# Kernel tuning notes

Measured on AMD Instinct MI355X. Metric: run time of the kernel, lower is better.

## Reference

```python
import jax, jax.numpy as jnp
import numpy as np

WS = 8          # window_size
NH = 8          # num_heads
VD = 512        # values_dim
CD = 128        # coords_dim
INNER = 512     # inner_ratio * values_dim
E = INNER // NH # head_dim = 64
B, Hh, Ww_ = 2, 224, 224

# relative position indices (static)
_idx = np.array([[x, y] for x in range(WS) for y in range(WS)])
_rel = _idx[None, :, :] - _idx[:, None, :] + WS - 1  # (WS^2, WS^2, 2)
REL0 = jnp.asarray(_rel[:, :, 0])
REL1 = jnp.asarray(_rel[:, :, 1])

# shifted-window masks (static)
_s = WS * (WS // 2)
_rm = np.zeros((WS * WS, WS * WS), np.float32)
_rm[-_s:, :-_s] = -np.inf
_rm[:-_s, -_s:] = -np.inf
_cm = _rm.reshape(WS, WS, WS, WS).transpose(1, 0, 3, 2).reshape(WS * WS, WS * WS)
ROW_MASK = jnp.asarray(_rm)
COL_MASK = jnp.asarray(_cm)


def _rmsnorm(x, g, eps=1e-6):
    return x * g * jax.lax.rsqrt(jnp.mean(x * x, axis=-1, keepdims=True) + eps)


def _to_windows(x, b, Wh, Ww):
    # x: (b, hp, wp, INNER) with channel layout (e H) (head fastest)
    x = x.reshape(b, Wh, WS, Ww, WS, E, NH)
    return x.transpose(0, 6, 1, 3, 2, 4, 5).reshape(b, NH, Wh, Ww, WS * WS, E)


def setup_inputs() -> dict:
    key = jax.random.key(0)
    ks = jax.random.split(key, 8)
    s = 0.02
    return {
        "embedded_values": jax.random.normal(ks[0], (B, Hh, Ww_, VD), jnp.float32),
        "embedded_coords": jax.random.normal(ks[1], (B, Hh, Ww_, CD), jnp.float32),
        "Wqk_v": jax.random.normal(ks[2], (VD, 2 * INNER), jnp.float32) * s,
        "bqk_v": jnp.zeros((2 * INNER,), jnp.float32),
        "g_v": jnp.ones((2 * INNER,), jnp.float32),
        "Wv": jax.random.normal(ks[3], (VD, INNER), jnp.float32) * s,
        "bv": jnp.zeros((INNER,), jnp.float32),
        "Wqk_c": jax.random.normal(ks[4], (CD, 2 * INNER), jnp.float32) * s,
        "bqk_c": jnp.zeros((2 * INNER,), jnp.float32),
        "g_c": jnp.ones((2 * INNER,), jnp.float32),
        "pos_emb": jax.random.normal(ks[5], (2 * WS - 1, 2 * WS - 1), jnp.float32),
        "Wout": jax.random.normal(ks[6], (INNER, VD), jnp.float32) * s,
        "bout": jnp.zeros((VD,), jnp.float32),
    }


def reference(embedded_values, embedded_coords, Wqk_v, bqk_v, g_v, Wv, bv,
              Wqk_c, bqk_c, g_c, pos_emb, Wout, bout):
    b, h, w, _ = embedded_values.shape
    # projections; torch concat then rearrange '(d k)' k=3 interleaves channels -> reshape (..., INNER, 3)
    vqk = _rmsnorm(embedded_values @ Wqk_v + bqk_v, g_v)          # (b,h,w,2*INNER)
    vval = embedded_values @ Wv + bv                               # (b,h,w,INNER)
    v = jnp.concatenate([vqk, vval], axis=-1).reshape(b, h, w, INNER, 3)
    c = _rmsnorm(embedded_coords @ Wqk_c + bqk_c, g_c).reshape(b, h, w, INNER, 2)

    pad_h = (-h) % WS
    pad_w = (-w) % WS
    v = jnp.pad(v, ((0, 0), (0, pad_h), (0, pad_w), (0, 0), (0, 0)))
    c = jnp.pad(c, ((0, 0), (0, pad_h), (0, pad_w), (0, 0), (0, 0)))
    # shifted=True: roll windows by half window (no inverse roll in original)
    v = jnp.roll(v, (-(WS // 2), -(WS // 2)), axis=(1, 2))
    c = jnp.roll(c, (-(WS // 2), -(WS // 2)), axis=(1, 2))

    hp, wp = h + pad_h, w + pad_w
    Wh, Ww = hp // WS, wp // WS
    qv = _to_windows(v[..., 0], b, Wh, Ww)
    kv = _to_windows(v[..., 1], b, Wh, Ww)
    vv = _to_windows(v[..., 2], b, Wh, Ww)
    qc = _to_windows(c[..., 0], b, Wh, Ww)
    kc = _to_windows(c[..., 1], b, Wh, Ww)

    scale = float(E) ** 0.5
    dots = (jnp.einsum('bhijpe,bhijqe->bhijpq', qv, kv)
            + jnp.einsum('bhijpe,bhijqe->bhijpq', qc, kc)) / scale
    dots = dots + pos_emb[REL0, REL1]
    # shifted-window masks on last window row / column
    dots = dots.at[:, :, -1, :].add(ROW_MASK)
    dots = dots.at[:, :, :, -1].add(COL_MASK)

    attn = jax.nn.softmax(dots, axis=-1)
    y = jnp.einsum('bhijpq,bhijqe->bhijpe', attn, vv)
    # un-window; output channel layout is (H e) (head slow)
    y = y.reshape(b, NH, Wh, Ww, WS, WS, E).transpose(0, 2, 4, 3, 5, 1, 6)
    y = y.reshape(b, hp, wp, INNER)[:, :h, :w, :]
    return y @ Wout + bout
```

## Files before the change

kernel.cpp:

```cpp
#include <hip/hip_runtime.h>


using u16 = unsigned short;
typedef short bf16x8 __attribute__((ext_vector_type(8)));
typedef float f32x4 __attribute__((ext_vector_type(4)));
typedef u16 u16x4 __attribute__((ext_vector_type(4)));
typedef u16 u16x8 __attribute__((ext_vector_type(8)));

__device__ __forceinline__ float bf2f(u16 v) {
  return __uint_as_float(((unsigned)v) << 16);
}
__device__ __forceinline__ u16 f2bf(float f) {
  unsigned u = __float_as_uint(f);
  u += 0x7fffu + ((u >> 16) & 1u);
  return (u16)(u >> 16);
}

__device__ __forceinline__ void gld16(const u16* g, u16* l) {
  __builtin_amdgcn_global_load_lds(
      (const __attribute__((address_space(1))) unsigned*)g,
      (__attribute__((address_space(3))) unsigned*)l, 16, 0, 0);
}

__global__ void conv_bf16(const float* __restrict__ in, u16* __restrict__ out) {
  size_t i = ((size_t)blockIdx.x * 256 + threadIdx.x) * 8;
  float4 a = *(const float4*)(in + i);
  float4 b = *(const float4*)(in + i + 4);
  u16x8 o;
  o[0] = f2bf(a.x); o[1] = f2bf(a.y); o[2] = f2bf(a.z); o[3] = f2bf(a.w);
  o[4] = f2bf(b.x); o[5] = f2bf(b.y); o[6] = f2bf(b.z); o[7] = f2bf(b.w);
  *(u16x8*)(out + i) = o;
}

__global__ void prep_wv(const float* __restrict__ Wqkv, const float* __restrict__ Wv,
                        u16* __restrict__ out) {
  int idx = blockIdx.x * 256 + threadIdx.x;
  if (idx >= 1536 * 512) return;
  int j = idx >> 9, kk = idx & 511;
  int t = j >> 9, rr = j & 511, nn = rr >> 6, e = rr & 63;
  int cc = 3 * (e * 8 + nn) + t;
  float v = (cc < 1024) ? Wqkv[kk * 1024 + cc] : Wv[kk * 512 + (cc - 1024)];
  out[idx] = f2bf(v);
}

__global__ void prep_wc(const float* __restrict__ W, u16* __restrict__ out) {
  int idx = blockIdx.x * 256 + threadIdx.x;
  if (idx >= 1024 * 128) return;
  int j = idx >> 7, kk = idx & 127;
  int t = j >> 9, rr = j & 511, nn = rr >> 6, e = rr & 63;
  int cc = 2 * (e * 8 + nn) + t;
  out[idx] = f2bf(W[kk * 1024 + cc]);
}

__global__ void prep_wout(const float* __restrict__ W, u16* __restrict__ out) {
  int idx = blockIdx.x * 256 + threadIdx.x;
  if (idx >= 512 * 512) return;
  int o = idx >> 9, kk = idx & 511;
  out[idx] = f2bf(W[kk * 512 + o]);
}

__global__ void prep_vec(const float* __restrict__ bqkv, const float* __restrict__ g_v,
                         const float* __restrict__ bv, const float* __restrict__ bqkc,
                         const float* __restrict__ g_c,
                         float* __restrict__ bpv, float* __restrict__ gAv, float* __restrict__ gBv,
                         float* __restrict__ bpc, float* __restrict__ gAc, float* __restrict__ gBc) {
  int j = blockIdx.x * 256 + threadIdx.x;
  if (j < 1536) {
    int t = j >> 9, rr = j & 511, nn = rr >> 6, e = rr & 63;
    int cc = 3 * (e * 8 + nn) + t;
    if (cc < 1024) { bpv[j] = bqkv[cc]; gAv[j] = g_v[cc]; gBv[j] = 0.f; }
    else           { bpv[j] = bv[cc - 1024]; gAv[j] = 0.f; gBv[j] = 1.f; }
  }
  if (j < 1024) {
    int t = j >> 9, rr = j & 511, nn = rr >> 6, e = rr & 63;
    int cc = 2 * (e * 8 + nn) + t;
    bpc[j] = bqkc[cc]; gAc[j] = g_c[cc]; gBc[j] = 0.f;
  }
}

__global__ void prep_biasT(const float* __restrict__ pe, float* __restrict__ bT) {
  int idx = blockIdx.x * 256 + threadIdx.x;
  if (idx >= 4 * 4096) return;
  int v = idx >> 12, q = (idx >> 6) & 63, p = idx & 63;
  int ap = p >> 3, bp = p & 7, aq = q >> 3, bq = q & 7;
  float val = pe[(aq - ap + 7) * 15 + (bq - bp + 7)];
  if ((v & 1) && ((ap >= 4) != (aq >= 4))) val = -1e30f;
  if ((v & 2) && ((bp >= 4) != (bq >= 4))) val = -1e30f;
  bT[idx] = val;
}

template<int N, int K, int MODE>
__global__ __launch_bounds__(256) void gemm_bt(
    const u16* __restrict__ A, const u16* __restrict__ Bt,
    const float* __restrict__ bias, void* __restrict__ outp,
    float* __restrict__ part, const float* __restrict__ gB) {
  constexpr int NCB = N / 128;
  const int bn = blockIdx.x, bm = blockIdx.y;
  const int tid = threadIdx.x;
  const int w = tid >> 6;
  const int lane = tid & 63;
  const int wr = w >> 1, wc = w & 1;
  const int g = lane >> 4, c = lane & 15;

  __shared__ u16 As[128 * 64];
  __shared__ u16 Bs[128 * 64];

  f32x4 acc[4][4] = {};
  const u16* Ag = A + (size_t)bm * 128 * K;
  const u16* Bg = Bt + (size_t)bn * 128 * K;

  const int lr = lane >> 3;
  const int lc = (lane & 7) * 8;

  for (int kt = 0; kt < K / 64; ++kt) {
    const int k0 = kt * 64;
#pragma unroll
    for (int i = 0; i < 4; ++i) {
      const int rbase = (w * 4 + i) * 8;
      gld16(Ag + (size_t)(rbase + lr) * K + k0 + lc, As + rbase * 64 + lane * 8);
      gld16(Bg + (size_t)(rbase + lr) * K + k0 + lc, Bs + rbase * 64 + lane * 8);
    }
    __syncthreads();
#pragma unroll
    for (int kk = 0; kk < 2; ++kk) {
      bf16x8 af[4], bfv[4];
#pragma unroll
      for (int mi = 0; mi < 4; ++mi)
        af[mi] = *(const bf16x8*)(As + (wr * 64 + mi * 16 + c) * 64 + kk * 32 + g * 8);
#pragma unroll
      for (int ni = 0; ni < 4; ++ni)
        bfv[ni] = *(const bf16x8*)(Bs + (wc * 64 + ni * 16 + c) * 64 + kk * 32 + g * 8);
#pragma unroll
      for (int mi = 0; mi < 4; ++mi)
#pragma unroll
        for (int ni = 0; ni < 4; ++ni)
          acc[mi][ni] = __builtin_amdgcn_mfma_f32_16x16x32_bf16(af[mi], bfv[ni], acc[mi][ni], 0, 0, 0);
    }
    __syncthreads();
  }

  const int rowbase = bm * 128 + wr * 64;
  const int colbase = bn * 128 + wc * 64;
  if constexpr (MODE == 0) {
    u16* O = (u16*)outp;
    float rowsq[4][4];
#pragma unroll
    for (int mi = 0; mi < 4; ++mi)
#pragma unroll
      for (int r = 0; r < 4; ++r) rowsq[mi][r] = 0.f;
#pragma unroll
    for (int ni = 0; ni < 4; ++ni) {
      const int col = colbase + ni * 16 + c;
      const float bb = bias[col];
      const float fl = (gB[col] == 0.f) ? 1.f : 0.f;
#pragma unroll
      for (int mi = 0; mi < 4; ++mi)
#pragma unroll
        for (int r = 0; r < 4; ++r) {
          float v = acc[mi][ni][r] + bb;
          O[(size_t)(rowbase + mi * 16 + g * 4 + r) * N + col] = f2bf(v);
          rowsq[mi][r] += fl * v * v;
        }
    }
#pragma unroll
    for (int mi = 0; mi < 4; ++mi)
#pragma unroll
      for (int r = 0; r < 4; ++r) {
        float s = rowsq[mi][r];
        s += __shfl_xor(s, 1); s += __shfl_xor(s, 2);
        s += __shfl_xor(s, 4); s += __shfl_xor(s, 8);
        rowsq[mi][r] = s;
      }
    __syncthreads();
    float* red = (float*)As;
    if (c == 0) {
#pragma unroll
      for (int mi = 0; mi < 4; ++mi)
#pragma unroll
        for (int r = 0; r < 4; ++r)
          red[wc * 128 + wr * 64 + mi * 16 + g * 4 + r] = rowsq[mi][r];
    }
    __syncthreads();
    if (tid < 128)
      part[(size_t)(bm * 128 + tid) * NCB + bn] = red[tid] + red[128 + tid];
  } else {
    float* O = (float*)outp;
#pragma unroll
    for (int ni = 0; ni < 4; ++ni) {
      const int col = colbase + ni * 16 + c;
      const float bb = bias[col];
#pragma unroll
      for (int mi = 0; mi < 4; ++mi)
#pragma unroll
        for (int r = 0; r < 4; ++r)
          O[(size_t)(rowbase + mi * 16 + g * 4 + r) * N + col] = acc[mi][ni][r] + bb;
    }
  }
}

__global__ void combine_scales(const float* __restrict__ pvp, const float* __restrict__ pcp,
                               float* __restrict__ sv, float* __restrict__ sc) {
  const int i = blockIdx.x * 256 + threadIdx.x;
  float s = 0.f;
#pragma unroll
  for (int k = 0; k < 12; ++k) s += pvp[(size_t)i * 12 + k];
  sv[i] = rsqrtf(s * (1.f / 1024.f) + 1e-6f);
  float s2 = 0.f;
#pragma unroll
  for (int k = 0; k < 8; ++k) s2 += pcp[(size_t)i * 8 + k];
  sc[i] = rsqrtf(s2 * (1.f / 1024.f) + 1e-6f);
}

__device__ __forceinline__ void store_norm(u16* dst, u16x8 raw, const float* gA,
                                           const float* gB, float s, int e0) {
  u16x8 o;
#pragma unroll
  for (int j = 0; j < 8; ++j) {
    float fac = gA[e0 + j] * s + gB[e0 + j];
    o[j] = f2bf(bf2f(raw[j]) * fac);
  }
  *(u16x8*)dst = o;
}

__global__ __launch_bounds__(64) void attn_kernel(
    const u16* __restrict__ Pv, const u16* __restrict__ Pc,
    const float* __restrict__ sv, const float* __restrict__ sc,
    const float* __restrict__ gAv, const float* __restrict__ gBv,
    const float* __restrict__ gAc, const float* __restrict__ gBc,
    const float* __restrict__ biasT, u16* __restrict__ Y) {
  const int l = threadIdx.x;
  int bx = blockIdx.x;
  const int wj = bx % 28; bx /= 28;
  const int wi = bx % 28; bx /= 28;
  const int n = bx & 7;
  const int bi = bx >> 3;

  const int g = l >> 4, c = l & 15;
  const int rr0 = l >> 3, rch = l & 7;

  __shared__ u16 Ka[64 * 72];
  __shared__ u16 Qa[64 * 72];
  __shared__ float gf[640];

  gf[l]       = gAv[n * 64 + l];          gf[64 + l]  = gBv[n * 64 + l];
  gf[128 + l] = gAv[512 + n * 64 + l];    gf[192 + l] = gBv[512 + n * 64 + l];
  gf[256 + l] = gAv[1024 + n * 64 + l];   gf[320 + l] = gBv[1024 + n * 64 + l];
  gf[384 + l] = gAc[n * 64 + l];          gf[448 + l] = gBc[n * 64 + l];
  gf[512 + l] = gAc[512 + n * 64 + l];    gf[576 + l] = gBc[512 + n * 64 + l];

  auto pixof = [&](int a, int b2) -> int {
    int y = wi * 8 + a + 4; if (y >= 224) y -= 224;
    int x = wj * 8 + b2 + 4; if (x >= 224) x -= 224;
    return (bi * 224 + y) * 224 + x;
  };

#pragma unroll
  for (int i = 0; i < 8; ++i) {
    const int pix = pixof(i, rr0);
    const float s = sv[pix];
    const u16* src = Pv + (size_t)pix * 1536 + n * 64 + rch * 8;
    u16x8 q = *(const u16x8*)src;
    u16x8 k = *(const u16x8*)(src + 512);
    store_norm(Qa + (i * 8 + rr0) * 72 + rch * 8, q, gf, gf + 64, s, rch * 8);
    store_norm(Ka + (i * 8 + rr0) * 72 + rch * 8, k, gf + 128, gf + 192, s, rch * 8);
  }

  f32x4 acc[4][4] = {};
  auto qk_accum = [&]() {
#pragma unroll
    for (int kk = 0; kk < 2; ++kk) {
      bf16x8 af[4], bq[4];
#pragma unroll
      for (int mi = 0; mi < 4; ++mi)
        af[mi] = *(const bf16x8*)(Ka + (mi * 16 + c) * 72 + kk * 32 + g * 8);
#pragma unroll
      for (int ni = 0; ni < 4; ++ni)
        bq[ni] = *(const bf16x8*)(Qa + (ni * 16 + c) * 72 + kk * 32 + g * 8);
#pragma unroll
      for (int mi = 0; mi < 4; ++mi)
#pragma unroll
        for (int ni = 0; ni < 4; ++ni)
          acc[mi][ni] = __builtin_amdgcn_mfma_f32_16x16x32_bf16(af[mi], bq[ni], acc[mi][ni], 0, 0, 0);
    }
  };
  qk_accum();

#pragma unroll
  for (int i = 0; i < 8; ++i) {
    const int pix = pixof(i, rr0);
    const float s = sc[pix];
    const u16* src = Pc + (size_t)pix * 1024 + n * 64 + rch * 8;
    u16x8 q = *(const u16x8*)src;
    u16x8 k = *(const u16x8*)(src + 512);
    store_norm(Qa + (i * 8 + rr0) * 72 + rch * 8, q, gf + 384, gf + 448, s, rch * 8);
    store_norm(Ka + (i * 8 + rr0) * 72 + rch * 8, k, gf + 512, gf + 576, s, rch * 8);
  }
  qk_accum();

  u16x8 vreg[8]; float vs_[8];
#pragma unroll
  for (int i = 0; i < 8; ++i) {
    const int pix = pixof(i, rr0);
    vs_[i] = sv[pix];
    vreg[i] = *(const u16x8*)(Pv + (size_t)pix * 1536 + 1024 + n * 64 + rch * 8);
  }

  const int variant = ((wi == 27) ? 1 : 0) | ((wj == 27) ? 2 : 0);
  const float* BT = biasT + variant * 4096;
#pragma unroll
  for (int mi = 0; mi < 4; ++mi)
#pragma unroll
    for (int ni = 0; ni < 4; ++ni)
#pragma unroll
      for (int r = 0; r < 4; ++r) {
        const int q = mi * 16 + g * 4 + r;
        const int p = ni * 16 + c;
        acc[mi][ni][r] = acc[mi][ni][r] * 0.125f + BT[q * 64 + p];
      }
  float rinv[4];
#pragma unroll
  for (int ni = 0; ni < 4; ++ni) {
    float m = -3.0e38f;
#pragma unroll
    for (int mi = 0; mi < 4; ++mi)
#pragma unroll
      for (int r = 0; r < 4; ++r) m = fmaxf(m, acc[mi][ni][r]);
    m = fmaxf(m, __shfl_xor(m, 16));
    m = fmaxf(m, __shfl_xor(m, 32));
    float ssum = 0.f;
#pragma unroll
    for (int mi = 0; mi < 4; ++mi)
#pragma unroll
      for (int r = 0; r < 4; ++r) {
        float e = __expf(acc[mi][ni][r] - m);
        acc[mi][ni][r] = e;
        ssum += e;
      }
    ssum += __shfl_xor(ssum, 16);
    ssum += __shfl_xor(ssum, 32);
    rinv[ni] = 1.f / ssum;
  }

  u16* Pl = Qa;
#pragma unroll
  for (int mi = 0; mi < 4; ++mi)
#pragma unroll
    for (int ni = 0; ni < 4; ++ni) {
      u16x4 pk;
#pragma unroll
      for (int r = 0; r < 4; ++r) pk[r] = f2bf(acc[mi][ni][r] * rinv[ni]);
      *(u16x4*)(Pl + (ni * 16 + c) * 72 + mi * 16 + g * 4) = pk;
    }
  u16* Vl = Ka;
#pragma unroll
  for (int i = 0; i < 8; ++i)
    store_norm(Vl + (i * 8 + rr0) * 72 + rch * 8, vreg[i], gf + 256, gf + 320, vs_[i], rch * 8);

  f32x4 ya[4][4] = {};
#pragma unroll
  for (int kk = 0; kk < 2; ++kk) {
    bf16x8 pa[4];
#pragma unroll
    for (int mi = 0; mi < 4; ++mi)
      pa[mi] = *(const bf16x8*)(Pl + (mi * 16 + c) * 72 + kk * 32 + g * 8);
#pragma unroll
    for (int ni = 0; ni < 4; ++ni) {
      u16x8 vtmp;
#pragma unroll
      for (int j = 0; j < 8; ++j)
        vtmp[j] = Vl[(kk * 32 + g * 8 + j) * 72 + ni * 16 + c];
      bf16x8 vb = *(bf16x8*)&vtmp;
#pragma unroll
      for (int mi = 0; mi < 4; ++mi)
        ya[mi][ni] = __builtin_amdgcn_mfma_f32_16x16x32_bf16(pa[mi], vb, ya[mi][ni], 0, 0, 0);
    }
  }

  u16* Yt = Qa;
#pragma unroll
  for (int mi = 0; mi < 4; ++mi)
#pragma unroll
    for (int ni = 0; ni < 4; ++ni) {
      u16x4 yk;
#pragma unroll
      for (int r = 0; r < 4; ++r) yk[r] = f2bf(ya[mi][ni][r]);
      *(u16x4*)(Yt + (ni * 16 + c) * 72 + mi * 16 + g * 4) = yk;
    }
  const int oy = wi * 8 + rr0, ox = wj * 8 + rch;
  u16* dst = Y + ((size_t)(bi * 224 + oy) * 224 + ox) * 512 + n * 64;
#pragma unroll
  for (int chn = 0; chn < 8; ++chn) {
    u16x8 row;
#pragma unroll
    for (int j = 0; j < 8; ++j) row[j] = Yt[(chn * 8 + j) * 72 + l];
    *(u16x8*)(dst + chn * 8) = row;
  }
}

extern "C" void kernel_launch(void* const* d_in, const int* in_sizes, int n_in,
                              void* d_out, int out_size, void* d_ws, size_t ws_size,
                              hipStream_t stream) {
  const float* ev   = (const float*)d_in[0];
  const float* ec   = (const float*)d_in[1];
  const float* Wqkv = (const float*)d_in[2];
  const float* bqkv = (const float*)d_in[3];
  const float* g_v  = (const float*)d_in[4];
  const float* Wv   = (const float*)d_in[5];
  const float* bv   = (const float*)d_in[6];
  const float* Wqkc = (const float*)d_in[7];
  const float* bqkc = (const float*)d_in[8];
  const float* g_c  = (const float*)d_in[9];
  const float* pe   = (const float*)d_in[10];
  const float* Wout = (const float*)d_in[11];
  const float* bout = (const float*)d_in[12];
  float* out = (float*)d_out;

  char* w = (char*)d_ws;
  auto take = [&](size_t b) { char* p = w; w += (b + 255) & ~(size_t)255; return p; };
  u16* Wvp   = (u16*)take(1536ull * 512 * 2);
  u16* Wcp   = (u16*)take(1024ull * 128 * 2);
  u16* Wob   = (u16*)take(512ull * 512 * 2);
  float* bpv = (float*)take(1536 * 4);
  float* gAv = (float*)take(1536 * 4);
  float* gBv = (float*)take(1536 * 4);
  float* bpc = (float*)take(1024 * 4);
  float* gAc = (float*)take(1024 * 4);
  float* gBc = (float*)take(1024 * 4);
  float* bT  = (float*)take(4 * 4096 * 4);
  u16* Pv    = (u16*)take(100352ull * 1536 * 2);
  u16* Pc    = (u16*)take(100352ull * 1024 * 2);
  float* pvp = (float*)take(100352ull * 12 * 4);
  float* pcp = (float*)take(100352ull * 8 * 4);
  float* sv  = (float*)take(100352ull * 4);
  float* sc  = (float*)take(100352ull * 4);
  u16* Yb    = (u16*)take(100352ull * 512 * 2);
  u16* evb   = Yb;
  u16* ecb   = (u16*)take(100352ull * 128 * 2);

  conv_bf16<<<25088, 256, 0, stream>>>(ev, evb);
  conv_bf16<<<6272, 256, 0, stream>>>(ec, ecb);
  prep_wv<<<3072, 256, 0, stream>>>(Wqkv, Wv, Wvp);
  prep_wc<<<512, 256, 0, stream>>>(Wqkc, Wcp);
  prep_wout<<<1024, 256, 0, stream>>>(Wout, Wob);
  prep_vec<<<6, 256, 0, stream>>>(bqkv, g_v, bv, bqkc, g_c, bpv, gAv, gBv, bpc, gAc, gBc);
  prep_biasT<<<64, 256, 0, stream>>>(pe, bT);

  gemm_bt<1536, 512, 0><<<dim3(12, 784), 256, 0, stream>>>(evb, Wvp, bpv, Pv, pvp, gBv);
  gemm_bt<1024, 128, 0><<<dim3(8, 784), 256, 0, stream>>>(ecb, Wcp, bpc, Pc, pcp, gBc);
  combine_scales<<<392, 256, 0, stream>>>(pvp, pcp, sv, sc);
  attn_kernel<<<12544, 64, 0, stream>>>(Pv, Pc, sv, sc, gAv, gBv, gAc, gBc, bT, Yb);
  gemm_bt<512, 512, 1><<<dim3(4, 784), 256, 0, stream>>>(Yb, Wob, bout, out, nullptr, nullptr);
}
```

Before: 852.7 us.

## Double-buffer GEMM LDS tiles and vectorize epilogue stores via swapped MFMA operands

The GEMM main loop now uses two 32-wide K buffers in LDS and issues the next tile's async global-to-LDS loads before computing on the current one, replacing the load-sync-compute pattern. The MFMA operands are swapped so each lane holds four consecutive output columns. This lets the epilogue write packed 4-element bf16 or float4 stores and cuts the row-sum-of-squares reduction to two shuffles. The cost is a halved K step, so there are more loop iterations and barriers. LDS reads in the 32-wide layout may also hit more bank conflicts.

```diff
diff --git a/kernel.cpp b/kernel.cpp
--- a/kernel.cpp
+++ b/kernel.cpp
@@ -95,6 +95,7 @@
     const float* __restrict__ bias, void* __restrict__ outp,
     float* __restrict__ part, const float* __restrict__ gB) {
   constexpr int NCB = N / 128;
+  constexpr int KT = K / 32;
   const int bn = blockIdx.x, bm = blockIdx.y;
   const int tid = threadIdx.x;
   const int w = tid >> 6;
@@ -102,40 +103,43 @@
   const int wr = w >> 1, wc = w & 1;
   const int g = lane >> 4, c = lane & 15;
 
-  __shared__ u16 As[128 * 64];
-  __shared__ u16 Bs[128 * 64];
+  __shared__ u16 As[2 * 4096];
+  __shared__ u16 Bs[2 * 4096];
 
   f32x4 acc[4][4] = {};
   const u16* Ag = A + (size_t)bm * 128 * K;
   const u16* Bg = Bt + (size_t)bn * 128 * K;
 
-  const int lr = lane >> 3;
-  const int lc = (lane & 7) * 8;
-
-  for (int kt = 0; kt < K / 64; ++kt) {
-    const int k0 = kt * 64;
-#pragma unroll
-    for (int i = 0; i < 4; ++i) {
-      const int rbase = (w * 4 + i) * 8;
-      gld16(Ag + (size_t)(rbase + lr) * K + k0 + lc, As + rbase * 64 + lane * 8);
-      gld16(Bg + (size_t)(rbase + lr) * K + k0 + lc, Bs + rbase * 64 + lane * 8);
-    }
-    __syncthreads();
-#pragma unroll
-    for (int kk = 0; kk < 2; ++kk) {
-      bf16x8 af[4], bfv[4];
-#pragma unroll
-      for (int mi = 0; mi < 4; ++mi)
-        af[mi] = *(const bf16x8*)(As + (wr * 64 + mi * 16 + c) * 64 + kk * 32 + g * 8);
+  auto stage = [&](int buf, int kt) {
+    const int k0 = kt * 32;
+#pragma unroll
+    for (int i = 0; i < 2; ++i) {
+      const int idx = i * 256 + tid;
+      const int row = idx >> 2, ch = (idx & 3) * 8;
+      gld16(Ag + (size_t)row * K + k0 + ch, As + buf * 4096 + idx * 8);
+      gld16(Bg + (size_t)row * K + k0 + ch, Bs + buf * 4096 + idx * 8);
+    }
+  };
+
+  stage(0, 0);
+  __syncthreads();
+
+  for (int kt = 0; kt < KT; ++kt) {
+    if (kt + 1 < KT) stage((kt + 1) & 1, kt + 1);
+    const u16* Ab = As + (kt & 1) * 4096;
+    const u16* Bb = Bs + (kt & 1) * 4096;
+    bf16x8 af[4], bfv[4];
+#pragma unroll
+    for (int mi = 0; mi < 4; ++mi)
+      af[mi] = *(const bf16x8*)(Ab + (wr * 64 + mi * 16 + c) * 32 + g * 8);
+#pragma unroll
+    for (int ni = 0; ni < 4; ++ni)
+      bfv[ni] = *(const bf16x8*)(Bb + (wc * 64 + ni * 16 + c) * 32 + g * 8);
+#pragma unroll
+    for (int mi = 0; mi < 4; ++mi)
 #pragma unroll
       for (int ni = 0; ni < 4; ++ni)
-        bfv[ni] = *(const bf16x8*)(Bs + (wc * 64 + ni * 16 + c) * 64 + kk * 32 + g * 8);
-#pragma unroll
-      for (int mi = 0; mi < 4; ++mi)
-#pragma unroll
-        for (int ni = 0; ni < 4; ++ni)
-          acc[mi][ni] = __builtin_amdgcn_mfma_f32_16x16x32_bf16(af[mi], bfv[ni], acc[mi][ni], 0, 0, 0);
-    }
+        acc[mi][ni] = __builtin_amdgcn_mfma_f32_16x16x32_bf16(bfv[ni], af[mi], acc[mi][ni], 0, 0, 0);
     __syncthreads();
   }
 
@@ -143,42 +147,38 @@
   const int colbase = bn * 128 + wc * 64;
   if constexpr (MODE == 0) {
     u16* O = (u16*)outp;
-    float rowsq[4][4];
-#pragma unroll
-    for (int mi = 0; mi < 4; ++mi)
-#pragma unroll
-      for (int r = 0; r < 4; ++r) rowsq[mi][r] = 0.f;
+    float rowsq[4] = {0.f, 0.f, 0.f, 0.f};
 #pragma unroll
     for (int ni = 0; ni < 4; ++ni) {
-      const int col = colbase + ni * 16 + c;
-      const float bb = bias[col];
-      const float fl = (gB[col] == 0.f) ? 1.f : 0.f;
+      const int col4 = colbase + ni * 16 + g * 4;
+      const float4 bb = *(const float4*)(bias + col4);
+      const float4 gb = *(const float4*)(gB + col4);
+#pragma unroll
+      for (int mi = 0; mi < 4; ++mi) {
+        const int row = rowbase + mi * 16 + c;
+        u16x4 pk;
+        float v0 = acc[mi][ni][0] + bb.x;
+        float v1 = acc[mi][ni][1] + bb.y;
+        float v2 = acc[mi][ni][2] + bb.z;
+        float v3 = acc[mi][ni][3] + bb.w;
+        pk[0] = f2bf(v0); pk[1] = f2bf(v1); pk[2] = f2bf(v2); pk[3] = f2bf(v3);
+        *(u16x4*)(O + (size_t)row * N + col4) = pk;
+        rowsq[mi] += (gb.x == 0.f ? v0 * v0 : 0.f) + (gb.y == 0.f ? v1 * v1 : 0.f)
+                   + (gb.z == 0.f ? v2 * v2 : 0.f) + (gb.w == 0.f ? v3 * v3 : 0.f);
+      }
+    }
+#pragma unroll
+    for (int mi = 0; mi < 4; ++mi) {
+      float s = rowsq[mi];
+      s += __shfl_xor(s, 16);
+      s += __shfl_xor(s, 32);
+      rowsq[mi] = s;
+    }
+    float* red = (float*)As;
+    if (g == 0) {
 #pragma unroll
       for (int mi = 0; mi < 4; ++mi)
-#pragma unroll
-        for (int r = 0; r < 4; ++r) {
-          float v = acc[mi][ni][r] + bb;
-          O[(size_t)(rowbase + mi * 16 + g * 4 + r) * N + col] = f2bf(v);
-          rowsq[mi][r] += fl * v * v;
-        }
-    }
-#pragma unroll
-    for (int mi = 0; mi < 4; ++mi)
-#pragma unroll
-      for (int r = 0; r < 4; ++r) {
-        float s = rowsq[mi][r];
-        s += __shfl_xor(s, 1); s += __shfl_xor(s, 2);
-        s += __shfl_xor(s, 4); s += __shfl_xor(s, 8);
-        rowsq[mi][r] = s;
-      }
-    __syncthreads();
-    float* red = (float*)As;
-    if (c == 0) {
-#pragma unroll
-      for (int mi = 0; mi < 4; ++mi)
-#pragma unroll
-        for (int r = 0; r < 4; ++r)
-          red[wc * 128 + wr * 64 + mi * 16 + g * 4 + r] = rowsq[mi][r];
+        red[wc * 128 + wr * 64 + mi * 16 + c] = rowsq[mi];
     }
     __syncthreads();
     if (tid < 128)
@@ -187,13 +187,18 @@
     float* O = (float*)outp;
 #pragma unroll
     for (int ni = 0; ni < 4; ++ni) {
-      const int col = colbase + ni * 16 + c;
-      const float bb = bias[col];
-#pragma unroll
-      for (int mi = 0; mi < 4; ++mi)
-#pragma unroll
-        for (int r = 0; r < 4; ++r)
-          O[(size_t)(rowbase + mi * 16 + g * 4 + r) * N + col] = acc[mi][ni][r] + bb;
+      const int col4 = colbase + ni * 16 + g * 4;
+      const float4 bb = *(const float4*)(bias + col4);
+#pragma unroll
+      for (int mi = 0; mi < 4; ++mi) {
+        const int row = rowbase + mi * 16 + c;
+        float4 o;
+        o.x = acc[mi][ni][0] + bb.x;
+        o.y = acc[mi][ni][1] + bb.y;
+        o.z = acc[mi][ni][2] + bb.z;
+        o.w = acc[mi][ni][3] + bb.w;
+        *(float4*)(O + (size_t)row * N + col4) = o;
+      }
     }
   }
 }
```

Measured after the change: 812.3 us. -4.7%, faster.
